# Kernel optimization log

Hardware: AMD Instinct MI355X
Metric: run time of the kernel (lower is better)

The kernel has to match this reference:

```python
import jax, jax.numpy as jnp
import numpy as np

B, T, D = 1, 2048, 4096
N, K, H = 32, 8, 128  # num_heads, num_kv_heads, head_dim
ROPE_BASE = 10000
SCALE_FACTOR = 1.0
EPS = 1e-6
NEG_INF = -1e9


def rms_norm(x):
    var = jnp.mean(jnp.square(x), axis=-1, keepdims=True)
    return x * jax.lax.rsqrt(var + EPS)


def apply_rope(x, positions, base_frequency, scale_factor=1.0):
    # x: [B, L, num_heads, H], positions: [B, L]
    head_dim = x.shape[-1]
    fraction = 2.0 * jnp.arange(head_dim // 2, dtype=jnp.float32) / head_dim
    timescale = base_frequency ** fraction  # [H/2]
    sinusoid = positions[..., None].astype(jnp.float32) / timescale  # [B,L,H/2]
    sinusoid = sinusoid[..., None, :] / scale_factor  # [B,L,1,H/2]
    sin, cos = jnp.sin(sinusoid), jnp.cos(sinusoid)
    x1, x2 = jnp.split(x, 2, axis=-1)
    return jnp.concatenate([x1 * cos - x2 * sin, x2 * cos + x1 * sin], axis=-1)


def setup_inputs() -> dict:
    key = jax.random.key(0)
    ks = jax.random.split(key, 7)
    x = jax.random.normal(ks[0], (B, T, D), dtype=jnp.float32)
    segment_pos = jnp.broadcast_to(jnp.arange(T, dtype=jnp.int32)[None, :], (B, T))
    causal = jnp.tril(jnp.ones((T, T), dtype=bool))
    attn_mask = jnp.where(causal, 0.0, NEG_INF).astype(jnp.float32)[None]  # [B,T,S]
    attn_mask = jnp.broadcast_to(attn_mask, (B, T, T))
    q_w = jax.random.normal(ks[1], (N, D, H), dtype=jnp.float32) * (D ** -0.5)
    kv_w = jax.random.normal(ks[2], (2, K, D, H), dtype=jnp.float32) * (D ** -0.5)
    o_w = jax.random.normal(ks[3], (N, H, D), dtype=jnp.float32) * ((N * H) ** -0.5)
    q_scale = jax.random.normal(ks[4], (H,), dtype=jnp.float32) * 0.02  # RMSNorm scale (zeros-init style)
    k_scale = jax.random.normal(ks[5], (H,), dtype=jnp.float32) * 0.02
    return {"x": x, "segment_pos": segment_pos, "attn_mask": attn_mask,
            "q_w": q_w, "kv_w": kv_w, "o_w": o_w,
            "q_scale": q_scale, "k_scale": k_scale}


def reference(x, segment_pos, attn_mask, q_w, kv_w, o_w, q_scale, k_scale):
    # Projections
    q = jnp.einsum('BTD,NDH->BTNH', x, q_w)          # [B,T,N,H]
    kv = jnp.einsum('BSD,CKDH->CBSKH', x, kv_w)      # [2,B,S,K,H]
    k, v = kv[0], kv[1]
    # QK RMSNorm (with scale, (1+scale) convention) and value RMSNorm (no scale)
    q = rms_norm(q) * (1.0 + q_scale)
    k = rms_norm(k) * (1.0 + k_scale)
    v = rms_norm(v)
    # RoPE (standard path: positions are [B,L])
    q = apply_rope(q, segment_pos, ROPE_BASE, SCALE_FACTOR)
    k = apply_rope(k, segment_pos, ROPE_BASE, SCALE_FACTOR)
    # GQA grouping: [B,T,K,G,H]
    G = N // K
    qg = q.reshape(B, T, K, G, H)
    attn_logits = jnp.einsum('btkgh,bskh->bkgts', qg, k)  # [B,K,G,T,S]
    attn_logits = attn_logits + attn_mask[:, None, None, :, :]
    attn_weights = jax.nn.softmax(attn_logits, axis=-1).astype(v.dtype)
    out = jnp.einsum('bkgts,bskh->btkgh', attn_weights, v)  # [B,T,K,G,H]
    out = out.reshape(B, T, N, H)
    return jnp.einsum('BTNH,NHD->BTD', out, o_w)
```

## Files before the change

kernel.cpp:

```cpp
#include <hip/hip_runtime.h>
#include <stdint.h>


typedef __bf16 bf16x8 __attribute__((ext_vector_type(8)));
typedef float  f32x4  __attribute__((ext_vector_type(4)));

__device__ __forceinline__ uint16_t f2bf(float f) {
    union { float f; uint32_t u; } v; v.f = f;
    uint32_t r = v.u + 0x7fffu + ((v.u >> 16) & 1u);
    return (uint16_t)(r >> 16);
}

__device__ __forceinline__ void gload_lds16(const void* g, void* l) {
    __builtin_amdgcn_global_load_lds(
        (const __attribute__((address_space(1))) uint32_t*)g,
        (__attribute__((address_space(3))) uint32_t*)l, 16, 0, 0);
}

__global__ __launch_bounds__(256) void k_cvt_x(const float* __restrict__ x,
                                               uint16_t* __restrict__ xb) {
    int i = (blockIdx.x * 256 + threadIdx.x) * 8;
    int r = i >> 12, k = i & 4095;
    float4 a = *(const float4*)(x + i);
    float4 b = *(const float4*)(x + i + 4);
    uint16_t tmp[8];
    tmp[0] = f2bf(a.x); tmp[1] = f2bf(a.y); tmp[2] = f2bf(a.z); tmp[3] = f2bf(a.w);
    tmp[4] = f2bf(b.x); tmp[5] = f2bf(b.y); tmp[6] = f2bf(b.z); tmp[7] = f2bf(b.w);
    int dst = r * 4096 + (k & ~63) + (((((k >> 3) & 7) ^ (r & 7))) << 3);
    *(uint4*)(xb + dst) = *(uint4*)tmp;
}

__global__ __launch_bounds__(256) void k_prep_wt(const float* __restrict__ qw,
                                                 const float* __restrict__ kvw,
                                                 uint16_t* __restrict__ Wt) {
    const int hx = blockIdx.x, dx = blockIdx.y, m = blockIdx.z;
    const float* src = (m < 32) ? (qw + (size_t)m * 524288)
                                : (kvw + (size_t)(m - 32) * 524288);
    __shared__ uint16_t tile[64][65];
    const int t = threadIdx.x, d0 = dx * 64, h0 = hx * 64;
#pragma unroll
    for (int i = 0; i < 16; ++i) {
        int idx = i * 256 + t, r = idx >> 6, c = idx & 63;
        tile[r][c] = f2bf(src[(size_t)(d0 + r) * 128 + h0 + c]);
    }
    __syncthreads();
#pragma unroll
    for (int it = 0; it < 2; ++it) {
        int slot = it * 256 + t, hr = slot >> 3, cl = slot & 7;
        int R = m * 128 + h0 + hr;
        uint16_t tmp[8];
#pragma unroll
        for (int e = 0; e < 8; ++e) tmp[e] = tile[cl * 8 + e][hr];
        *(uint4*)&Wt[(size_t)R * 4096 + d0 + ((cl ^ (R & 7)) << 3)] = *(uint4*)tmp;
    }
}

__global__ __launch_bounds__(256) void k_prep_ot(const float* __restrict__ ow,
                                                 uint16_t* __restrict__ Ot) {
    const int dx = blockIdx.x, hx = blockIdx.y, n = blockIdx.z;
    const float* src = ow + (size_t)n * 524288;
    __shared__ uint16_t tile[64][65];
    const int t = threadIdx.x, h0 = hx * 64, d0 = dx * 64;
#pragma unroll
    for (int i = 0; i < 16; ++i) {
        int idx = i * 256 + t, r = idx >> 6, c = idx & 63;
        tile[r][c] = f2bf(src[(size_t)(h0 + r) * 4096 + d0 + c]);
    }
    __syncthreads();
#pragma unroll
    for (int it = 0; it < 2; ++it) {
        int slot = it * 256 + t, dr = slot >> 3, cl = slot & 7;
        int R = d0 + dr;
        uint16_t tmp[8];
#pragma unroll
        for (int e = 0; e < 8; ++e) tmp[e] = tile[cl * 8 + e][dr];
        *(uint4*)&Ot[(size_t)R * 4096 + n * 128 + h0 + ((cl ^ (R & 7)) << 3)] = *(uint4*)tmp;
    }
}

#define PH_BAR do { asm volatile("" ::: "memory"); \
                    __builtin_amdgcn_s_barrier(); \
                    asm volatile("" ::: "memory"); } while (0)
#define WAIT_VM(N) do { asm volatile("s_waitcnt vmcnt(" #N ")" ::: "memory"); \
                        __builtin_amdgcn_sched_barrier(0); } while (0)
#define SCHED0 __builtin_amdgcn_sched_barrier(0)

__global__ __launch_bounds__(512, 2) void k_gemm_qkv(const uint16_t* __restrict__ A,
                                                     const uint16_t* __restrict__ Bt,
                                                     const int* __restrict__ pos,
                                                     const float* __restrict__ qs,
                                                     const float* __restrict__ ks,
                                                     uint16_t* __restrict__ Qg,
                                                     uint16_t* __restrict__ Kg,
                                                     uint16_t* __restrict__ Vg) {
    extern __shared__ __align__(16) char smem[];
    uint16_t* lds = (uint16_t*)smem;
    const int Kd = 4096;
    const int t = threadIdx.x, wid = t >> 6, lane = t & 63;
    const int l16 = lane & 15, quad = lane >> 4;
    const int wr = wid >> 2, wc = wid & 3;
    const int bx = blockIdx.x, bm0 = blockIdx.y * 256, bn0 = bx * 256;

    f32x4 acc[8][4];
    const f32x4 z4 = {0.f, 0.f, 0.f, 0.f};
#pragma unroll
    for (int i = 0; i < 8; ++i)
#pragma unroll
        for (int j = 0; j < 4; ++j) acc[i][j] = z4;

    const int r0 = wid * 16 + (lane >> 2), c4 = lane & 3;
    const int sw2 = (r0 >> 1) & 3, sw7 = r0 & 7;
    const int offK0 = (((c4 ^ sw2)) ^ sw7) * 8;
    const int offK1 = ((4 + (c4 ^ sw2)) ^ sw7) * 8;
    const uint16_t* pA0 = A + (size_t)(bm0 + r0) * Kd;
    const uint16_t* pA1 = pA0 + (size_t)128 * Kd;
    const uint16_t* pB0 = Bt + (size_t)(bn0 + r0) * Kd;
    const uint16_t* pB1 = pB0 + (size_t)128 * Kd;
    uint16_t* stA = lds + wid * 512;
    uint16_t* stB = lds + 32768 + wid * 512;

    const int sA = (l16 >> 1) & 3;
    const int rdA = (wr * 128 + l16) * 32 + ((quad ^ sA) << 3);
    const int rdB = 32768 + (wc * 64 + l16) * 32 + ((quad ^ sA) << 3);

    bf16x8 afA[4], afB[4], bfA[4], bfB[4];

#define STAGE_A(SLAB, OFF, TT) do { \
    gload_lds16(pA0 + (size_t)(TT) * 64 + (OFF), stA + (SLAB) * 8192); \
    gload_lds16(pA1 + (size_t)(TT) * 64 + (OFF), stA + (SLAB) * 8192 + 4096); } while (0)
#define STAGE_B(SLAB, OFF, TT) do { \
    gload_lds16(pB0 + (size_t)(TT) * 64 + (OFF), stB + (SLAB) * 8192); \
    gload_lds16(pB1 + (size_t)(TT) * 64 + (OFF), stB + (SLAB) * 8192 + 4096); } while (0)
#define RD_A(DST, SLAB, I0) do { _Pragma("unroll") \
    for (int i_ = 0; i_ < 4; ++i_) \
        DST[i_] = *(const bf16x8*)&lds[(SLAB) * 8192 + rdA + ((I0) + i_) * 512]; } while (0)
#define RD_B(DST, SLAB) do { _Pragma("unroll") \
    for (int j_ = 0; j_ < 4; ++j_) \
        DST[j_] = *(const bf16x8*)&lds[(SLAB) * 8192 + rdB + j_ * 512]; } while (0)
#define MFMA16(AF, BF, I0) do { __builtin_amdgcn_s_setprio(1); \
    _Pragma("unroll") for (int i_ = 0; i_ < 4; ++i_) \
        _Pragma("unroll") for (int j_ = 0; j_ < 4; ++j_) \
            acc[(I0) + i_][j_] = __builtin_amdgcn_mfma_f32_16x16x32_bf16(AF[i_], BF[j_], acc[(I0) + i_][j_], 0, 0, 0); \
    __builtin_amdgcn_s_setprio(0); } while (0)

#define TILE(TT, BUF) do { \
    RD_A(afB, 2*(BUF), 4); \
    WAIT_VM(4); \
    STAGE_A(2*((BUF)^1)+1, offK1, (TT)+1); \
    SCHED0; MFMA16(afA, bfA, 0); PH_BAR; \
    RD_A(afA, 2*(BUF)+1, 0); RD_B(bfB, 2*(BUF)+1); \
    STAGE_B(2*((BUF)^1)+1, offK1, (TT)+1); \
    SCHED0; MFMA16(afB, bfA, 4); PH_BAR; \
    RD_A(afB, 2*(BUF)+1, 4); \
    WAIT_VM(4); \
    STAGE_A(2*(BUF), offK0, (TT)+2); \
    SCHED0; MFMA16(afA, bfB, 0); PH_BAR; \
    RD_A(afA, 2*((BUF)^1), 0); RD_B(bfA, 2*((BUF)^1)); \
    STAGE_B(2*(BUF), offK0, (TT)+2); \
    SCHED0; MFMA16(afB, bfB, 4); PH_BAR; \
} while (0)

    STAGE_A(0, offK0, 0); STAGE_B(0, offK0, 0);
    STAGE_A(1, offK1, 0); STAGE_B(1, offK1, 0);
    STAGE_A(2, offK0, 1); STAGE_B(2, offK0, 1);
    WAIT_VM(8);
    PH_BAR;
    RD_A(afA, 0, 0); RD_B(bfA, 0);

#pragma unroll 1
    for (int Ti = 0; Ti < 31; ++Ti) {
        TILE(2 * Ti, 0);
        TILE(2 * Ti + 1, 1);
    }

    RD_A(afB, 0, 4); WAIT_VM(4); STAGE_A(3, offK1, 63);
    SCHED0; MFMA16(afA, bfA, 0); PH_BAR;
    RD_A(afA, 1, 0); RD_B(bfB, 1); STAGE_B(3, offK1, 63);
    SCHED0; MFMA16(afB, bfA, 4); PH_BAR;
    RD_A(afB, 1, 4); WAIT_VM(4);
    SCHED0; MFMA16(afA, bfB, 0); PH_BAR;
    RD_A(afA, 2, 0); RD_B(bfA, 2);
    SCHED0; MFMA16(afB, bfB, 4); PH_BAR;
    RD_A(afB, 2, 4); WAIT_VM(0);
    SCHED0; MFMA16(afA, bfA, 0); PH_BAR;
    RD_A(afA, 3, 0); RD_B(bfB, 3);
    SCHED0; MFMA16(afB, bfA, 4); PH_BAR;
    RD_A(afB, 3, 4);
    SCHED0; MFMA16(afA, bfB, 0); PH_BAR;
    SCHED0; MFMA16(afB, bfB, 4);

#undef TILE
#undef MFMA16
#undef RD_B
#undef RD_A
#undef STAGE_B
#undef STAGE_A

    float* X   = (float*)smem;
    float* ssq = (float*)(smem + 133120);

#pragma unroll
    for (int i = 0; i < 8; ++i)
#pragma unroll
        for (int r = 0; r < 4; ++r) {
            float s = 0.f;
#pragma unroll
            for (int j = 0; j < 4; ++j) s += acc[i][j][r] * acc[i][j][r];
            s += __shfl_xor(s, 1); s += __shfl_xor(s, 2);
            s += __shfl_xor(s, 4); s += __shfl_xor(s, 8);
            if (l16 == 0)
                ssq[(wr * 128 + i * 16 + quad * 4 + r) * 4 + (wc >> 1) * 2 + (wc & 1)] = s;
        }
    __syncthreads();

    const int cat = (bx < 16) ? 0 : (bx < 20 ? 1 : 2);
    float s1 = 0.f, s2 = 0.f, invts = 0.f;
    if (cat < 2) {
        const float* sc = cat ? ks : qs;
        s1 = 1.0f + sc[lane];
        s2 = 1.0f + sc[lane + 64];
        invts = exp2f((float)lane * -0.20762050593046014f);
    }

#pragma unroll
    for (int pass = 0; pass < 2; ++pass) {
        if (wr == pass) {
#pragma unroll
            for (int i = 0; i < 8; ++i)
#pragma unroll
                for (int j = 0; j < 4; ++j)
#pragma unroll
                    for (int r = 0; r < 4; ++r)
                        X[(i * 16 + quad * 4 + r) * 260 + wc * 64 + j * 16 + l16] = acc[i][j][r];
        }
        __syncthreads();
        for (int rr = 0; rr < 16; ++rr) {
            const int lrow = wid * 16 + rr;
            const int grow = bm0 + pass * 128 + lrow;
            float sn = 0.f, cs = 0.f;
            if (cat < 2) {
                float ang = (float)pos[grow] * invts;
                __sincosf(ang, &sn, &cs);
            }
#pragma unroll
            for (int hh = 0; hh < 2; ++hh) {
                const int sb = (pass * 128 + lrow) * 4 + hh * 2;
                float rn = rsqrtf((ssq[sb] + ssq[sb + 1]) * 0.0078125f + 1e-6f);
                float x1 = X[lrow * 260 + hh * 128 + lane];
                float x2 = X[lrow * 260 + hh * 128 + 64 + lane];
                if (cat < 2) {
                    float y1 = x1 * rn * s1, y2 = x2 * rn * s2;
                    X[lrow * 260 + hh * 128 + lane]      = y1 * cs - y2 * sn;
                    X[lrow * 260 + hh * 128 + 64 + lane] = y2 * cs + y1 * sn;
                } else {
                    X[lrow * 260 + hh * 128 + lane]      = x1 * rn;
                    X[lrow * 260 + hh * 128 + 64 + lane] = x2 * rn;
                }
            }
        }
        __syncthreads();
        if (cat == 2) {
#pragma unroll
            for (int it = 0; it < 8; ++it) {
                int slot = it * 512 + t, hh = slot >> 11, rem = slot & 2047;
                int h = rem >> 4, sc2 = rem & 15;
                uint16_t tmp[8];
#pragma unroll
                for (int e = 0; e < 8; ++e)
                    tmp[e] = f2bf(X[(sc2 * 8 + e) * 260 + hh * 128 + h]);
                int n = bx * 2 + hh;
                *(uint4*)&Vg[((size_t)(n - 40) * 128 + h) * 2048 + (bm0 + pass * 128)
                             + ((sc2 ^ (h & 15)) << 3)] = *(uint4*)tmp;
            }
        } else {
#pragma unroll
            for (int it = 0; it < 8; ++it) {
                int slot = it * 512 + t, hh = slot >> 11, rem = slot & 2047;
                int lrow = rem >> 4, c = rem & 15;
                int tg = bm0 + pass * 128 + lrow, n = bx * 2 + hh;
                f32x4 a = *(f32x4*)&X[lrow * 260 + hh * 128 + c * 8];
                f32x4 b = *(f32x4*)&X[lrow * 260 + hh * 128 + c * 8 + 4];
                uint16_t tmp[8];
#pragma unroll
                for (int e = 0; e < 4; ++e) { tmp[e] = f2bf(a[e]); tmp[4 + e] = f2bf(b[e]); }
                if (cat == 0)
                    *(uint4*)&Qg[((size_t)n * 2048 + tg) * 128 + c * 8] = *(uint4*)tmp;
                else
                    *(uint4*)&Kg[((size_t)(n - 32) * 2048 + tg) * 128
                                 + ((c ^ (tg & 15)) << 3)] = *(uint4*)tmp;
            }
        }
        __syncthreads();
    }
}

__global__ __launch_bounds__(512, 2) void k_gemm2p(const uint16_t* __restrict__ A,
                                                   const uint16_t* __restrict__ Bt,
                                                   float* __restrict__ C) {
    extern __shared__ __align__(16) char smem2[];
    uint16_t* lds = (uint16_t*)smem2;
    const int Kd = 4096, Nn = 4096;
    const int t = threadIdx.x, wid = t >> 6, lane = t & 63;
    const int l16 = lane & 15, quad = lane >> 4;
    const int wr = wid >> 1, wc = wid & 1;
    const int bm0 = blockIdx.y * 256, bn0 = blockIdx.x * 128;

    f32x4 acc[4][4];
    const f32x4 z4 = {0.f, 0.f, 0.f, 0.f};
#pragma unroll
    for (int i = 0; i < 4; ++i)
#pragma unroll
        for (int j = 0; j < 4; ++j) acc[i][j] = z4;

    const int r0 = wid * 16 + (lane >> 2), c4 = lane & 3;
    const int sw2 = (r0 >> 1) & 3, sw7 = r0 & 7;
    const int offK0 = ((c4 ^ sw2) ^ sw7) * 8;
    const int offK1 = ((4 + (c4 ^ sw2)) ^ sw7) * 8;
    const uint16_t* pA0 = A + (size_t)(bm0 + r0) * Kd;
    const uint16_t* pA1 = pA0 + (size_t)128 * Kd;
    const uint16_t* pB0 = Bt + (size_t)(bn0 + r0) * Kd;
    uint16_t* stA = lds + wid * 512;
    uint16_t* stB = lds + 49152 + wid * 512;

    const int sA = (l16 >> 1) & 3;
    const int rdA = (wr * 64 + l16) * 32 + ((quad ^ sA) << 3);
    const int rdB = 49152 + (wc * 64 + l16) * 32 + ((quad ^ sA) << 3);

    bf16x8 afA[4], afB[4], bfA[4], bfB[4];

#define G2_STAGE(SLAB, OFF, TT) do { \
    gload_lds16(pA0 + (size_t)(TT) * 64 + (OFF), stA + (SLAB) * 8192); \
    gload_lds16(pA1 + (size_t)(TT) * 64 + (OFF), stA + (SLAB) * 8192 + 4096); \
    gload_lds16(pB0 + (size_t)(TT) * 64 + (OFF), stB + (SLAB) * 4096); } while (0)
#define G2_RD(AD, BD, CS) do { _Pragma("unroll") \
    for (int i_ = 0; i_ < 4; ++i_) \
        AD[i_] = *(const bf16x8*)&lds[(CS) * 8192 + rdA + i_ * 512]; \
    _Pragma("unroll") for (int j_ = 0; j_ < 4; ++j_) \
        BD[j_] = *(const bf16x8*)&lds[(CS) * 4096 + rdB + j_ * 512]; } while (0)
#define G2_MFMA(AF, BF) do { __builtin_amdgcn_s_setprio(1); \
    _Pragma("unroll") for (int i_ = 0; i_ < 4; ++i_) \
        _Pragma("unroll") for (int j_ = 0; j_ < 4; ++j_) \
            acc[i_][j_] = __builtin_amdgcn_mfma_f32_16x16x32_bf16(AF[i_], BF[j_], acc[i_][j_], 0, 0, 0); \
    __builtin_amdgcn_s_setprio(0); } while (0)

#define G2_PH(RA, RB, CSN, SST, OFF, TT, MA, MB) do { \
    G2_RD(RA, RB, CSN); \
    WAIT_VM(3); \
    G2_STAGE(SST, OFF, TT); \
    SCHED0; G2_MFMA(MA, MB); PH_BAR; } while (0)

    G2_STAGE(0, offK0, 0);
    G2_STAGE(1, offK1, 0);
    G2_STAGE(2, offK0, 1);
    G2_STAGE(3, offK1, 1);
    WAIT_VM(6);
    PH_BAR;
    G2_RD(afA, bfA, 0);

#pragma unroll 1
    for (int m = 0; m < 20; ++m) {
        G2_PH(afB, bfB, 1, 4, offK0, 3*m + 2, afA, bfA);
        G2_PH(afA, bfA, 2, 5, offK1, 3*m + 2, afB, bfB);
        G2_PH(afB, bfB, 3, 0, offK0, 3*m + 3, afA, bfA);
        G2_PH(afA, bfA, 4, 1, offK1, 3*m + 3, afB, bfB);
        G2_PH(afB, bfB, 5, 2, offK0, 3*m + 4, afA, bfA);
        G2_PH(afA, bfA, 0, 3, offK1, 3*m + 4, afB, bfB);
    }
    G2_PH(afB, bfB, 1, 4, offK0, 62, afA, bfA);
    G2_PH(afA, bfA, 2, 5, offK1, 62, afB, bfB);
    G2_PH(afB, bfB, 3, 0, offK0, 63, afA, bfA);
    G2_PH(afA, bfA, 4, 1, offK1, 63, afB, bfB);
    G2_RD(afB, bfB, 5); WAIT_VM(3); SCHED0; G2_MFMA(afA, bfA); PH_BAR;
    G2_RD(afA, bfA, 0); WAIT_VM(0); SCHED0; G2_MFMA(afB, bfB); PH_BAR;
    G2_RD(afB, bfB, 1);              SCHED0; G2_MFMA(afA, bfA); PH_BAR;
    SCHED0; G2_MFMA(afB, bfB);

#undef G2_PH
#undef G2_MFMA
#undef G2_RD
#undef G2_STAGE

#pragma unroll
    for (int i = 0; i < 4; ++i)
#pragma unroll
        for (int j = 0; j < 4; ++j) {
            int row = bm0 + wr * 64 + i * 16 + quad * 4;
            int col = bn0 + wc * 64 + j * 16 + l16;
            float* cp = C + (size_t)row * Nn + col;
            cp[0]              = acc[i][j][0];
            cp[(size_t)Nn]     = acc[i][j][1];
            cp[2 * (size_t)Nn] = acc[i][j][2];
            cp[3 * (size_t)Nn] = acc[i][j][3];
        }
}

__global__ __launch_bounds__(256) void k_attn(const uint16_t* __restrict__ Q,
                                              const uint16_t* __restrict__ K,
                                              const uint16_t* __restrict__ Vt,
                                              uint16_t* __restrict__ att) {
    __shared__ uint16_t sK[128 * 128];
    __shared__ uint16_t sV[128 * 128];
    const int p = blockIdx.x, n = blockIdx.y, kk = n >> 2;
    const int t = threadIdx.x, wave = t >> 6, lane = t & 63;
    const int l16 = lane & 15, quad = lane >> 4;
    const f32x4 z4 = {0.f, 0.f, 0.f, 0.f};

    const uint16_t* Kbase = K  + ((size_t)kk * 2048 + wave * 32 + (lane >> 4)) * 128 + (lane & 15) * 8;
    const uint16_t* Vbase = Vt + ((size_t)kk * 128  + wave * 32 + (lane >> 4)) * 2048 + (lane & 15) * 8;

    for (int half = 0; half < 2; ++half) {
        const int qt = half ? (31 - p) : p;
        const int q0 = qt * 64;
        const int nk = (qt >> 1) + 1;

        bf16x8 qf[4];
#pragma unroll
        for (int kc = 0; kc < 4; ++kc)
            qf[kc] = *(const bf16x8*)(Q + (size_t)(n * 2048 + q0 + wave * 16 + l16) * 128 + kc * 32 + quad * 8);

        f32x4 O[8];
#pragma unroll
        for (int h = 0; h < 8; ++h) O[h] = z4;
        float mrow[4], lrow[4];
#pragma unroll
        for (int r = 0; r < 4; ++r) { mrow[r] = -INFINITY; lrow[r] = 0.f; }

        for (int st = 0; st < nk; ++st) {
            const int s0 = st * 128;
            __syncthreads();
#pragma unroll
            for (int j = 0; j < 8; ++j) {
                gload_lds16(Kbase + (size_t)(s0 + j * 4) * 128, &sK[(wave * 32 + j * 4) * 128]);
                gload_lds16(Vbase + (size_t)j * 4 * 2048 + s0,  &sV[(wave * 32 + j * 4) * 128]);
            }
            __syncthreads();

            f32x4 S[8];
#pragma unroll
            for (int jn = 0; jn < 8; ++jn) S[jn] = z4;
#pragma unroll
            for (int jn = 0; jn < 8; ++jn) {
                int krow = jn * 16 + l16;
#pragma unroll
                for (int kc = 0; kc < 4; ++kc) {
                    bf16x8 b = *(const bf16x8*)&sK[krow * 128 + (((kc * 4 + quad) ^ l16) << 3)];
                    S[jn] = __builtin_amdgcn_mfma_f32_16x16x32_bf16(qf[kc], b, S[jn], 0, 0, 0);
                }
            }
            if (st == nk - 1) {
#pragma unroll
                for (int jn = 0; jn < 8; ++jn) {
                    int sc = s0 + jn * 16 + l16;
#pragma unroll
                    for (int r = 0; r < 4; ++r) {
                        int mr = q0 + wave * 16 + quad * 4 + r;
                        if (sc > mr) S[jn][r] = -INFINITY;
                    }
                }
            }
            float alpha[4];
#pragma unroll
            for (int r = 0; r < 4; ++r) {
                float mx = S[0][r];
#pragma unroll
                for (int jn = 1; jn < 8; ++jn) mx = fmaxf(mx, S[jn][r]);
                mx = fmaxf(mx, __shfl_xor(mx, 1));
                mx = fmaxf(mx, __shfl_xor(mx, 2));
                mx = fmaxf(mx, __shfl_xor(mx, 4));
                mx = fmaxf(mx, __shfl_xor(mx, 8));
                float mnew = fmaxf(mrow[r], mx);
                float a = __expf(mrow[r] - mnew);
                mrow[r] = mnew;
                float sum = 0.f;
#pragma unroll
                for (int jn = 0; jn < 8; ++jn) {
                    float e = __expf(S[jn][r] - mnew);
                    S[jn][r] = e;
                    sum += e;
                }
                sum += __shfl_xor(sum, 1);
                sum += __shfl_xor(sum, 2);
                sum += __shfl_xor(sum, 4);
                sum += __shfl_xor(sum, 8);
                lrow[r] = lrow[r] * a + sum;
                alpha[r] = a;
            }
#pragma unroll
            for (int h = 0; h < 8; ++h)
#pragma unroll
                for (int r = 0; r < 4; ++r) O[h][r] *= alpha[r];

            __syncthreads();
#pragma unroll
            for (int jn = 0; jn < 8; ++jn)
#pragma unroll
                for (int r = 0; r < 4; ++r) {
                    int prow = wave * 16 + quad * 4 + r;
                    int pcol = jn * 16 + l16;
                    sK[prow * 128 + ((pcol & 7) | ((((pcol >> 3) ^ prow) & 15) << 3))]
                        = f2bf(S[jn][r]);
                }
            bf16x8 pf[4];
#pragma unroll
            for (int ksv = 0; ksv < 4; ++ksv)
                pf[ksv] = *(const bf16x8*)&sK[(wave * 16 + l16) * 128 + (((ksv * 4 + quad) ^ l16) << 3)];
#pragma unroll
            for (int hj = 0; hj < 8; ++hj) {
                int vrow = hj * 16 + l16;
#pragma unroll
                for (int ksv = 0; ksv < 4; ++ksv) {
                    bf16x8 b = *(const bf16x8*)&sV[vrow * 128 + (((ksv * 4 + quad) ^ l16) << 3)];
                    O[hj] = __builtin_amdgcn_mfma_f32_16x16x32_bf16(pf[ksv], b, O[hj], 0, 0, 0);
                }
            }
        }

        __syncthreads();
        uint16_t* sO = &sK[wave * 2112];
        float inv[4];
#pragma unroll
        for (int r = 0; r < 4; ++r) inv[r] = 1.0f / lrow[r];
#pragma unroll
        for (int hj = 0; hj < 8; ++hj)
#pragma unroll
            for (int r = 0; r < 4; ++r)
                sO[(quad * 4 + r) * 132 + hj * 16 + l16] = f2bf(O[hj][r] * inv[r]);
#pragma unroll
        for (int it = 0; it < 4; ++it) {
            int slot = it * 64 + lane, rloc = slot >> 4, cl = slot & 15;
            bf16x8 v = *(const bf16x8*)&sO[rloc * 132 + cl * 8];
            int R = q0 + wave * 16 + rloc;
            size_t dst = (size_t)R * 4096 + n * 128 + ((cl & 8) << 3) + (((cl & 7) ^ (R & 7)) << 3);
            *(uint4*)&att[dst] = *(uint4*)&v;
        }
    }
}

extern "C" void kernel_launch(void* const* d_in, const int* in_sizes, int n_in,
                              void* d_out, int out_size, void* d_ws, size_t ws_size,
                              hipStream_t stream) {
    const float* x   = (const float*)d_in[0];
    const int*   sp  = (const int*)d_in[1];
    const float* qw  = (const float*)d_in[3];
    const float* kvw = (const float*)d_in[4];
    const float* ow  = (const float*)d_in[5];
    const float* qsc = (const float*)d_in[6];
    const float* ksc = (const float*)d_in[7];
    float* out = (float*)d_out;

    char* ws = (char*)d_ws;
    uint16_t* xb   = (uint16_t*)(ws);
    uint16_t* Wt   = (uint16_t*)(ws + (size_t)(16u << 20));
    uint16_t* Qb   = (uint16_t*)(ws + (size_t)(64u << 20));
    uint16_t* Kb   = (uint16_t*)(ws + (size_t)(80u << 20));
    uint16_t* Vtb  = (uint16_t*)(ws + (size_t)(84u << 20));
    uint16_t* att  = (uint16_t*)(ws);
    uint16_t* Ot   = (uint16_t*)(ws + (size_t)(16u << 20));

    static bool attr_done = false;
    if (!attr_done) {
        hipFuncSetAttribute(reinterpret_cast<const void*>(k_gemm_qkv),
                            hipFuncAttributeMaxDynamicSharedMemorySize, 137216);
        hipFuncSetAttribute(reinterpret_cast<const void*>(k_gemm2p),
                            hipFuncAttributeMaxDynamicSharedMemorySize, 147456);
        attr_done = true;
    }

    k_cvt_x    <<<4096, 256, 0, stream>>>(x, xb);
    k_prep_wt  <<<dim3(2, 64, 48), 256, 0, stream>>>(qw, kvw, Wt);
    k_gemm_qkv <<<dim3(24, 8), 512, 137216, stream>>>(xb, Wt, sp, qsc, ksc, Qb, Kb, Vtb);
    k_prep_ot  <<<dim3(64, 2, 32), 256, 0, stream>>>(ow, Ot);
    k_attn     <<<dim3(16, 32), 256, 0, stream>>>(Qb, Kb, Vtb, att);
    k_gemm2p   <<<dim3(32, 8), 512, 147456, stream>>>(att, Ot, out);
}
```

Baseline: 514.4 us.

## Restructure attention into 512-thread blocks sharing K/V tiles across paired query tiles

The attention kernel now launches 8x32 blocks of 512 threads. Two wave groups process a causally balanced pair of 128-row query tiles (p and 15-p) and share each K/V tile staged into dynamic LDS. Each wave handles 32 query rows with two accumulator sets, so every K/V LDS read feeds twice as many MFMAs, and the softmax probabilities go to a per-wave LDS buffer instead of overwriting sK. This is meant to cut global K/V traffic and LDS reads per FLOP. In exchange it raises register pressure, may cause spills, and leaves the shorter-tile group idle during the later iterations of each block.

```diff
diff --git a/kernel.cpp b/kernel.cpp
--- a/kernel.cpp
+++ b/kernel.cpp
@@ -394,142 +394,158 @@
         }
 }
 
-__global__ __launch_bounds__(256) void k_attn(const uint16_t* __restrict__ Q,
-                                              const uint16_t* __restrict__ K,
-                                              const uint16_t* __restrict__ Vt,
-                                              uint16_t* __restrict__ att) {
-    __shared__ uint16_t sK[128 * 128];
-    __shared__ uint16_t sV[128 * 128];
+__global__ __launch_bounds__(512, 2) void k_attn(const uint16_t* __restrict__ Q,
+                                                 const uint16_t* __restrict__ K,
+                                                 const uint16_t* __restrict__ Vt,
+                                                 uint16_t* __restrict__ att) {
+    extern __shared__ __align__(16) char asmem[];
+    uint16_t* sK = (uint16_t*)asmem;
+    uint16_t* sV = sK + 16384;
+    uint16_t* sP = sK + 32768;
     const int p = blockIdx.x, n = blockIdx.y, kk = n >> 2;
-    const int t = threadIdx.x, wave = t >> 6, lane = t & 63;
+    const int t = threadIdx.x, wid = t >> 6, lane = t & 63;
     const int l16 = lane & 15, quad = lane >> 4;
+    const int grp = wid >> 2, wsub = wid & 3;
+    const int nk_a = p + 1, nk_b = 16 - p;
+    const int nk_w = grp ? nk_b : nk_a;
+    const int qbase = (grp ? (15 - p) * 128 : p * 128) + wsub * 32;
     const f32x4 z4 = {0.f, 0.f, 0.f, 0.f};
 
-    const uint16_t* Kbase = K  + ((size_t)kk * 2048 + wave * 32 + (lane >> 4)) * 128 + (lane & 15) * 8;
-    const uint16_t* Vbase = Vt + ((size_t)kk * 128  + wave * 32 + (lane >> 4)) * 2048 + (lane & 15) * 8;
-
-    for (int half = 0; half < 2; ++half) {
-        const int qt = half ? (31 - p) : p;
-        const int q0 = qt * 64;
-        const int nk = (qt >> 1) + 1;
-
-        bf16x8 qf[4];
-#pragma unroll
-        for (int kc = 0; kc < 4; ++kc)
-            qf[kc] = *(const bf16x8*)(Q + (size_t)(n * 2048 + q0 + wave * 16 + l16) * 128 + kc * 32 + quad * 8);
-
-        f32x4 O[8];
-#pragma unroll
-        for (int h = 0; h < 8; ++h) O[h] = z4;
-        float mrow[4], lrow[4];
-#pragma unroll
-        for (int r = 0; r < 4; ++r) { mrow[r] = -INFINITY; lrow[r] = 0.f; }
-
-        for (int st = 0; st < nk; ++st) {
-            const int s0 = st * 128;
-            __syncthreads();
-#pragma unroll
-            for (int j = 0; j < 8; ++j) {
-                gload_lds16(Kbase + (size_t)(s0 + j * 4) * 128, &sK[(wave * 32 + j * 4) * 128]);
-                gload_lds16(Vbase + (size_t)j * 4 * 2048 + s0,  &sV[(wave * 32 + j * 4) * 128]);
-            }
-            __syncthreads();
-
-            f32x4 S[8];
-#pragma unroll
-            for (int jn = 0; jn < 8; ++jn) S[jn] = z4;
+    const uint16_t* Kbase = K  + ((size_t)kk * 2048 + wid * 16 + (lane >> 4)) * 128 + (lane & 15) * 8;
+    const uint16_t* Vbase = Vt + ((size_t)kk * 128  + wid * 16 + (lane >> 4)) * 2048 + (lane & 15) * 8;
+    uint16_t* sPw = sP + wid * 32 * 128;
+
+    bf16x8 qf0[4], qf1[4];
+#pragma unroll
+    for (int kc = 0; kc < 4; ++kc) {
+        qf0[kc] = *(const bf16x8*)(Q + (size_t)(n * 2048 + qbase + l16) * 128 + kc * 32 + quad * 8);
+        qf1[kc] = *(const bf16x8*)(Q + (size_t)(n * 2048 + qbase + 16 + l16) * 128 + kc * 32 + quad * 8);
+    }
+
+    f32x4 O0[8], O1[8];
+#pragma unroll
+    for (int h = 0; h < 8; ++h) { O0[h] = z4; O1[h] = z4; }
+    float mrow0[4], lrow0[4], mrow1[4], lrow1[4];
+#pragma unroll
+    for (int r = 0; r < 4; ++r) {
+        mrow0[r] = -INFINITY; lrow0[r] = 0.f;
+        mrow1[r] = -INFINITY; lrow1[r] = 0.f;
+    }
+
+#define SM_SET(S, MR, LR, OO, ROWB, MASKED, S0V) do { \
+    if (MASKED) { \
+        _Pragma("unroll") for (int jn_ = 0; jn_ < 8; ++jn_) { \
+            int sc_ = (S0V) + jn_ * 16 + l16; \
+            _Pragma("unroll") for (int r_ = 0; r_ < 4; ++r_) { \
+                int mr_ = (ROWB) + quad * 4 + r_; \
+                if (sc_ > mr_) S[jn_][r_] = -INFINITY; \
+            } \
+        } \
+    } \
+    float alpha_[4]; \
+    _Pragma("unroll") for (int r_ = 0; r_ < 4; ++r_) { \
+        float mx_ = S[0][r_]; \
+        _Pragma("unroll") for (int jn_ = 1; jn_ < 8; ++jn_) mx_ = fmaxf(mx_, S[jn_][r_]); \
+        mx_ = fmaxf(mx_, __shfl_xor(mx_, 1)); \
+        mx_ = fmaxf(mx_, __shfl_xor(mx_, 2)); \
+        mx_ = fmaxf(mx_, __shfl_xor(mx_, 4)); \
+        mx_ = fmaxf(mx_, __shfl_xor(mx_, 8)); \
+        float mn_ = fmaxf(MR[r_], mx_); \
+        float a_ = __expf(MR[r_] - mn_); \
+        MR[r_] = mn_; \
+        float sum_ = 0.f; \
+        _Pragma("unroll") for (int jn_ = 0; jn_ < 8; ++jn_) { \
+            float e_ = __expf(S[jn_][r_] - mn_); \
+            S[jn_][r_] = e_; \
+            sum_ += e_; \
+        } \
+        sum_ += __shfl_xor(sum_, 1); \
+        sum_ += __shfl_xor(sum_, 2); \
+        sum_ += __shfl_xor(sum_, 4); \
+        sum_ += __shfl_xor(sum_, 8); \
+        LR[r_] = LR[r_] * a_ + sum_; \
+        alpha_[r_] = a_; \
+    } \
+    _Pragma("unroll") for (int h_ = 0; h_ < 8; ++h_) \
+        _Pragma("unroll") for (int r_ = 0; r_ < 4; ++r_) OO[h_][r_] *= alpha_[r_]; \
+} while (0)
+
+    for (int st = 0; st < nk_b; ++st) {
+        const int s0 = st * 128;
+        __syncthreads();
+#pragma unroll
+        for (int j = 0; j < 4; ++j) {
+            gload_lds16(Kbase + (size_t)(s0 + j * 4) * 128, &sK[(wid * 16 + j * 4) * 128]);
+            gload_lds16(Vbase + (size_t)(j * 4) * 2048 + s0, &sV[(wid * 16 + j * 4) * 128]);
+        }
+        __syncthreads();
+
+        if (st < nk_w) {
+            f32x4 S0[8], S1[8];
+#pragma unroll
+            for (int jn = 0; jn < 8; ++jn) { S0[jn] = z4; S1[jn] = z4; }
 #pragma unroll
             for (int jn = 0; jn < 8; ++jn) {
                 int krow = jn * 16 + l16;
 #pragma unroll
                 for (int kc = 0; kc < 4; ++kc) {
                     bf16x8 b = *(const bf16x8*)&sK[krow * 128 + (((kc * 4 + quad) ^ l16) << 3)];
-                    S[jn] = __builtin_amdgcn_mfma_f32_16x16x32_bf16(qf[kc], b, S[jn], 0, 0, 0);
+                    S0[jn] = __builtin_amdgcn_mfma_f32_16x16x32_bf16(qf0[kc], b, S0[jn], 0, 0, 0);
+                    S1[jn] = __builtin_amdgcn_mfma_f32_16x16x32_bf16(qf1[kc], b, S1[jn], 0, 0, 0);
                 }
             }
-            if (st == nk - 1) {
-#pragma unroll
-                for (int jn = 0; jn < 8; ++jn) {
-                    int sc = s0 + jn * 16 + l16;
-#pragma unroll
-                    for (int r = 0; r < 4; ++r) {
-                        int mr = q0 + wave * 16 + quad * 4 + r;
-                        if (sc > mr) S[jn][r] = -INFINITY;
-                    }
+            const int masked = (st == nk_w - 1);
+            SM_SET(S0, mrow0, lrow0, O0, qbase, masked, s0);
+            SM_SET(S1, mrow1, lrow1, O1, qbase + 16, masked, s0);
+
+#pragma unroll
+            for (int jn = 0; jn < 8; ++jn)
+#pragma unroll
+                for (int r = 0; r < 4; ++r) {
+                    int prow = quad * 4 + r;
+                    int pcol = jn * 16 + l16;
+                    int off = (pcol & 7) | ((((pcol >> 3) ^ prow) & 15) << 3);
+                    sPw[prow * 128 + off]        = f2bf(S0[jn][r]);
+                    sPw[(16 + prow) * 128 + off] = f2bf(S1[jn][r]);
                 }
-            }
-            float alpha[4];
-#pragma unroll
-            for (int r = 0; r < 4; ++r) {
-                float mx = S[0][r];
-#pragma unroll
-                for (int jn = 1; jn < 8; ++jn) mx = fmaxf(mx, S[jn][r]);
-                mx = fmaxf(mx, __shfl_xor(mx, 1));
-                mx = fmaxf(mx, __shfl_xor(mx, 2));
-                mx = fmaxf(mx, __shfl_xor(mx, 4));
-                mx = fmaxf(mx, __shfl_xor(mx, 8));
-                float mnew = fmaxf(mrow[r], mx);
-                float a = __expf(mrow[r] - mnew);
-                mrow[r] = mnew;
-                float sum = 0.f;
-#pragma unroll
-                for (int jn = 0; jn < 8; ++jn) {
-                    float e = __expf(S[jn][r] - mnew);
-                    S[jn][r] = e;
-                    sum += e;
-                }
-                sum += __shfl_xor(sum, 1);
-                sum += __shfl_xor(sum, 2);
-                sum += __shfl_xor(sum, 4);
-                sum += __shfl_xor(sum, 8);
-                lrow[r] = lrow[r] * a + sum;
-                alpha[r] = a;
-            }
-#pragma unroll
-            for (int h = 0; h < 8; ++h)
-#pragma unroll
-                for (int r = 0; r < 4; ++r) O[h][r] *= alpha[r];
-
-            __syncthreads();
-#pragma unroll
-            for (int jn = 0; jn < 8; ++jn)
-#pragma unroll
-                for (int r = 0; r < 4; ++r) {
-                    int prow = wave * 16 + quad * 4 + r;
-                    int pcol = jn * 16 + l16;
-                    sK[prow * 128 + ((pcol & 7) | ((((pcol >> 3) ^ prow) & 15) << 3))]
-                        = f2bf(S[jn][r]);
-                }
-            bf16x8 pf[4];
-#pragma unroll
-            for (int ksv = 0; ksv < 4; ++ksv)
-                pf[ksv] = *(const bf16x8*)&sK[(wave * 16 + l16) * 128 + (((ksv * 4 + quad) ^ l16) << 3)];
+            bf16x8 pf0[4], pf1[4];
+#pragma unroll
+            for (int ksv = 0; ksv < 4; ++ksv) {
+                pf0[ksv] = *(const bf16x8*)&sPw[l16 * 128 + (((ksv * 4 + quad) ^ l16) << 3)];
+                pf1[ksv] = *(const bf16x8*)&sPw[(16 + l16) * 128 + (((ksv * 4 + quad) ^ l16) << 3)];
+            }
 #pragma unroll
             for (int hj = 0; hj < 8; ++hj) {
                 int vrow = hj * 16 + l16;
 #pragma unroll
                 for (int ksv = 0; ksv < 4; ++ksv) {
                     bf16x8 b = *(const bf16x8*)&sV[vrow * 128 + (((ksv * 4 + quad) ^ l16) << 3)];
-                    O[hj] = __builtin_amdgcn_mfma_f32_16x16x32_bf16(pf[ksv], b, O[hj], 0, 0, 0);
+                    O0[hj] = __builtin_amdgcn_mfma_f32_16x16x32_bf16(pf0[ksv], b, O0[hj], 0, 0, 0);
+                    O1[hj] = __builtin_amdgcn_mfma_f32_16x16x32_bf16(pf1[ksv], b, O1[hj], 0, 0, 0);
                 }
             }
         }
-
-        __syncthreads();
-        uint16_t* sO = &sK[wave * 2112];
+    }
+#undef SM_SET
+
+#pragma unroll
+    for (int set = 0; set < 2; ++set) {
         float inv[4];
 #pragma unroll
-        for (int r = 0; r < 4; ++r) inv[r] = 1.0f / lrow[r];
+        for (int r = 0; r < 4; ++r)
+            inv[r] = 1.0f / (set ? lrow1[r] : lrow0[r]);
 #pragma unroll
         for (int hj = 0; hj < 8; ++hj)
 #pragma unroll
-            for (int r = 0; r < 4; ++r)
-                sO[(quad * 4 + r) * 132 + hj * 16 + l16] = f2bf(O[hj][r] * inv[r]);
+            for (int r = 0; r < 4; ++r) {
+                float v = (set ? O1[hj][r] : O0[hj][r]) * inv[r];
+                sPw[(quad * 4 + r) * 132 + hj * 16 + l16] = f2bf(v);
+            }
 #pragma unroll
         for (int it = 0; it < 4; ++it) {
             int slot = it * 64 + lane, rloc = slot >> 4, cl = slot & 15;
-            bf16x8 v = *(const bf16x8*)&sO[rloc * 132 + cl * 8];
-            int R = q0 + wave * 16 + rloc;
+            bf16x8 v = *(const bf16x8*)&sPw[rloc * 132 + cl * 8];
+            int R = qbase + set * 16 + rloc;
             size_t dst = (size_t)R * 4096 + n * 128 + ((cl & 8) << 3) + (((cl & 7) ^ (R & 7)) << 3);
             *(uint4*)&att[dst] = *(uint4*)&v;
         }
@@ -563,6 +579,8 @@
                             hipFuncAttributeMaxDynamicSharedMemorySize, 137216);
         hipFuncSetAttribute(reinterpret_cast<const void*>(k_gemm2p),
                             hipFuncAttributeMaxDynamicSharedMemorySize, 147456);
+        hipFuncSetAttribute(reinterpret_cast<const void*>(k_attn),
+                            hipFuncAttributeMaxDynamicSharedMemorySize, 131072);
         attr_done = true;
     }
 
@@ -570,6 +588,6 @@
     k_prep_wt  <<<dim3(2, 64, 48), 256, 0, stream>>>(qw, kvw, Wt);
     k_gemm_qkv <<<dim3(24, 8), 512, 137216, stream>>>(xb, Wt, sp, qsc, ksc, Qb, Kb, Vtb);
     k_prep_ot  <<<dim3(64, 2, 32), 256, 0, stream>>>(ow, Ot);
-    k_attn     <<<dim3(16, 32), 256, 0, stream>>>(Qb, Kb, Vtb, att);
+    k_attn     <<<dim3(8, 32), 512, 131072, stream>>>(Qb, Kb, Vtb, att);
     k_gemm2p   <<<dim3(32, 8), 512, 147456, stream>>>(att, Ot, out);
 }
```

Measured after the change: 521.9 us. About the same (+1.5%).
